# Optimization experiments

Measured on AMD Instinct MI355X. Metric: run time of the kernel, lower is better.

## Reference

```python
import jax, jax.numpy as jnp
import numpy as np

CELLS = 56
EPS = 1e-9

def setup_inputs() -> dict:
    key = jax.random.key(0)
    k1, k2 = jax.random.split(key)
    B = 512
    F = CELLS * CELLS * 15  # 47040 floats per sample
    output = jax.random.uniform(k1, (B, F), dtype=jnp.float32)
    target = jax.random.uniform(k2, (B, F), dtype=jnp.float32)
    return {"output": output, "target": target}

def reference(output, target):
    B = output.shape[0]
    # reshape flat vector into [B, cells^2, 15] slots: x,y,w,h,conf,classes[5:14]
    o = output.reshape(B, CELLS * CELLS, 15)
    t = target.reshape(B, CELLS * CELLS, 15)
    # coordinate loss: only x (slice [i*15 : i*15+1]) plus sqrt(w)/sqrt(h) terms
    coord = (o[..., 0] - t[..., 0]) ** 2 \
          + (jnp.sqrt(o[..., 2]) - jnp.sqrt(t[..., 2])) ** 2 \
          + (jnp.sqrt(o[..., 3]) - jnp.sqrt(t[..., 3])) ** 2
    # binary cross-entropy on confidence (slot 4)
    conf = -(t[..., 4] * jnp.log(o[..., 4] + EPS)
             + (1.0 - t[..., 4]) * jnp.log(1.0 - o[..., 4] + EPS))
    # class loss: sum of squared diffs over slots 5:14 (9 elements)
    cls = jnp.sum((t[..., 5:14] - o[..., 5:14]) ** 2, axis=-1)
    # cell is counted only if output x-coordinate is nonzero (torch.is_nonzero gate)
    mask = o[..., 0] != 0
    per_cell = jnp.where(mask, coord + conf + cls, 0.0)
    return jnp.sum(per_cell)
```

## Files before the change

### kernel.cpp

```cpp
#include <hip/hip_runtime.h>


#define EPSF 1e-9f
#define LN2F 0.69314718055994530942f

__device__ __forceinline__ float bce_of(float ox, float tx) {
    const float l1 = __log2f(ox + EPSF);
    const float l2 = __log2f((1.f - ox) + EPSF);
    return -LN2F * (tx * l1 + (1.f - tx) * l2);
}

__global__ __launch_bounds__(256, 4) void yolo_loss_fast(
    const float* __restrict__ o, const float* __restrict__ t,
    float* __restrict__ out_sum)
{
    const int tid = threadIdx.x;
    const unsigned T   = gridDim.x * 256u;
    const unsigned idx = blockIdx.x * 256u + (unsigned)tid;
    const float4* o4 = (const float4*)o;
    const float4* t4 = (const float4*)t;

    float4 ob[8], tb[8];
    float  gl[8], gh[8];
    unsigned sl[8];
    #pragma unroll
    for (int k = 0; k < 8; ++k) {
        const unsigned i  = idx + (unsigned)k * T;
        const unsigned e0 = i * 4u;
        const unsigned c0 = e0 / 15u;
        const unsigned c3 = (e0 + 3u) / 15u;
        sl[k] = e0 - c0 * 15u;
        ob[k] = o4[i];
        tb[k] = t4[i];
        gl[k] = o[c0 * 15u];
        gh[k] = o[c3 * 15u];
    }
    __builtin_amdgcn_sched_barrier(0);

    float acc = 0.f;
    #pragma unroll
    for (int k = 0; k < 8; ++k) {
        const unsigned s0 = sl[k];
        const float glo = gl[k], ghi = gh[k];
        const float oe[4] = {ob[k].x, ob[k].y, ob[k].z, ob[k].w};
        const float te[4] = {tb[k].x, tb[k].y, tb[k].z, tb[k].w};

        bool is4[4];
        #pragma unroll
        for (int j = 0; j < 4; ++j) {
            const unsigned s = s0 + (unsigned)j;
            is4[j] = (s == 4u) | (s == 19u);
        }
        float oc = oe[3], tc = te[3];
        #pragma unroll
        for (int j = 2; j >= 0; --j) { oc = is4[j] ? oe[j] : oc; tc = is4[j] ? te[j] : tc; }
        const float bce = bce_of(oc, tc);

        #pragma unroll
        for (int j = 0; j < 4; ++j) {
            unsigned s = s0 + (unsigned)j;
            const bool wrap = s >= 15u;
            s = wrap ? s - 15u : s;
            const float gate = wrap ? ghi : glo;
            const float ox = oe[j], tx = te[j];

            const float d  = ox - tx;
            const float sq = d * d;
            const float s23 = (ox + tx) - 2.f * __builtin_amdgcn_sqrtf(ox * tx);

            float c = ((s == 2u) | (s == 3u)) ? s23 : sq;
            c = is4[j] ? bce : c;
            c = ((s == 1u) | (s == 14u)) ? 0.f : c;
            c = (gate != 0.f) ? c : 0.f;
            acc += c;
        }
    }

    #pragma unroll
    for (int off = 32; off; off >>= 1) acc += __shfl_down(acc, off, 64);
    __shared__ float wsum[4];
    if ((tid & 63) == 0) wsum[tid >> 6] = acc;
    __syncthreads();
    if (tid == 0) atomicAdd(out_sum, wsum[0] + wsum[1] + wsum[2] + wsum[3]);
}

__global__ __launch_bounds__(256) void yolo_loss_generic(
    const float* __restrict__ o, const float* __restrict__ t,
    float* __restrict__ out_sum, int n4, int n)
{
    const int tid = threadIdx.x;
    const int stride = gridDim.x * 256;
    const float4* o4 = (const float4*)o;
    const float4* t4 = (const float4*)t;
    float acc = 0.f;

    for (int i = blockIdx.x * 256 + tid; i < n4; i += stride) {
        const float4 ov = o4[i];
        const float4 tv = t4[i];
        const unsigned e0 = (unsigned)i * 4u;
        const unsigned c0 = e0 / 15u;
        const unsigned c3 = (e0 + 3u) / 15u;
        const unsigned s0 = e0 - c0 * 15u;
        const float glo = o[c0 * 15u], ghi = o[c3 * 15u];
        const float oe[4] = {ov.x, ov.y, ov.z, ov.w};
        const float te[4] = {tv.x, tv.y, tv.z, tv.w};
        #pragma unroll
        for (int j = 0; j < 4; ++j) {
            unsigned s = s0 + (unsigned)j;
            const bool wrap = s >= 15u;
            s = wrap ? s - 15u : s;
            const float gate = wrap ? ghi : glo;
            const float ox = oe[j], tx = te[j];
            const float d = ox - tx;
            const float sq = d * d;
            const float s23 = (ox + tx) - 2.f * __builtin_amdgcn_sqrtf(ox * tx);
            float c = ((s == 2u) | (s == 3u)) ? s23 : sq;
            c = (s == 4u) ? bce_of(ox, tx) : c;
            c = ((s == 1u) | (s == 14u)) ? 0.f : c;
            c = (gate != 0.f) ? c : 0.f;
            acc += c;
        }
    }
    const int tail0 = n4 * 4;
    if (blockIdx.x == 0 && tid < n - tail0) {
        const unsigned e = (unsigned)(tail0 + tid);
        const unsigned cell = e / 15u;
        const unsigned s = e - cell * 15u;
        const float gate = o[cell * 15u];
        const float ox = o[e], tx = t[e];
        const float d = ox - tx;
        float c = d * d;
        c = ((s == 2u) | (s == 3u)) ? (ox + tx) - 2.f * __builtin_amdgcn_sqrtf(ox * tx) : c;
        c = (s == 4u) ? bce_of(ox, tx) : c;
        c = ((s == 1u) | (s == 14u)) ? 0.f : c;
        c = (gate != 0.f) ? c : 0.f;
        acc += c;
    }
    #pragma unroll
    for (int off = 32; off; off >>= 1) acc += __shfl_down(acc, off, 64);
    __shared__ float wsum[4];
    if ((tid & 63) == 0) wsum[tid >> 6] = acc;
    __syncthreads();
    if (tid == 0) atomicAdd(out_sum, wsum[0] + wsum[1] + wsum[2] + wsum[3]);
}

extern "C" void kernel_launch(void* const* d_in, const int* in_sizes, int n_in,
                              void* d_out, int out_size, void* d_ws, size_t ws_size,
                              hipStream_t stream) {
    const float* o = (const float*)d_in[0];
    const float* t = (const float*)d_in[1];
    float* out = (float*)d_out;
    const int n = in_sizes[0];
    const int n4 = n / 4;

    hipMemsetAsync(out, 0, sizeof(float), stream);

    if ((n % 4 == 0) && (n4 % (256 * 8) == 0)) {
        const int grid = n4 / (256 * 8);
        yolo_loss_fast<<<grid, 256, 0, stream>>>(o, t, out);
    } else {
        yolo_loss_generic<<<2940, 256, 0, stream>>>(o, t, out, n4, n);
    }
}
```

Before: 205.9 us.

## Map each wavefront to whole 15-float cells and fetch gates via shuffles

Each wavefront now processes windows of 60 float4s (240 floats, sixteen cells), so the per-lane slot pattern and cell boundaries are fixed and computed once per thread instead of per element. The scattered gate loads of each cell's x value are replaced by cross-lane shuffles from the lane that already holds that value. The grid is also fixed to 1792 blocks of 7 iterations with 7 waves per SIMD. The cost is that 4 of 64 lanes sit idle, and the fast path is tied to one exact input size.

```diff
diff --git a/kernel.cpp b/kernel.cpp
--- a/kernel.cpp
+++ b/kernel.cpp
@@ -3,6 +3,13 @@
 
 #define EPSF 1e-9f
 #define LN2F 0.69314718055994530942f
+
+#define GRID    1792
+#define KITERS  7
+#define BLK_E   (KITERS * 1920)
+#define FAST_N  (GRID * BLK_E)
+
+typedef float f32x4 __attribute__((ext_vector_type(4)));
 
 __device__ __forceinline__ float bce_of(float ox, float tx) {
     const float l1 = __log2f(ox + EPSF);
@@ -10,70 +17,85 @@
     return -LN2F * (tx * l1 + (1.f - tx) * l2);
 }
 
-__global__ __launch_bounds__(256, 4) void yolo_loss_fast(
+__global__ __launch_bounds__(256, 7) void yolo_loss_wave(
     const float* __restrict__ o, const float* __restrict__ t,
     float* __restrict__ out_sum)
 {
-    const int tid = threadIdx.x;
-    const unsigned T   = gridDim.x * 256u;
-    const unsigned idx = blockIdx.x * 256u + (unsigned)tid;
-    const float4* o4 = (const float4*)o;
-    const float4* t4 = (const float4*)t;
+    const int tid  = threadIdx.x;
+    const int lane = tid & 63;
+    const int wv   = tid >> 6;
+    const bool act = lane < 60;
 
-    float4 ob[8], tb[8];
-    float  gl[8], gh[8];
-    unsigned sl[8];
+    const f32x4* o4 = (const f32x4*)o;
+    const f32x4* t4 = (const f32x4*)t;
+
+    const unsigned le  = 4u * (unsigned)lane;
+    const unsigned c0r = le / 15u;
+    const unsigned c3r = (le + 3u) / 15u;
+    const unsigned s0  = le - c0r * 15u;
+    const int d_lo = (int)((15u * c0r) >> 2);
+    const int d_hi = (int)((15u * c3r) >> 2);
+    const unsigned j_own = (le + 14u) / 15u;
+    const unsigned gpos  = 15u * j_own - le;
+
+    bool is4[4], ksq[4], kz[4], wr[4];
     #pragma unroll
-    for (int k = 0; k < 8; ++k) {
-        const unsigned i  = idx + (unsigned)k * T;
-        const unsigned e0 = i * 4u;
-        const unsigned c0 = e0 / 15u;
-        const unsigned c3 = (e0 + 3u) / 15u;
-        sl[k] = e0 - c0 * 15u;
-        ob[k] = o4[i];
-        tb[k] = t4[i];
-        gl[k] = o[c0 * 15u];
-        gh[k] = o[c3 * 15u];
+    for (int j = 0; j < 4; ++j) {
+        const unsigned s = s0 + (unsigned)j;
+        is4[j] = (s == 4u);
+        ksq[j] = (s == 2u) | (s == 3u) | (s == 17u);
+        kz [j] = (s == 1u) | (s == 14u) | (s == 16u);
+        wr [j] = (s >= 15u);
     }
-    __builtin_amdgcn_sched_barrier(0);
 
-    float acc = 0.f;
-    #pragma unroll
-    for (int k = 0; k < 8; ++k) {
-        const unsigned s0 = sl[k];
-        const float glo = gl[k], ghi = gh[k];
-        const float oe[4] = {ob[k].x, ob[k].y, ob[k].z, ob[k].w};
-        const float te[4] = {tb[k].x, tb[k].y, tb[k].z, tb[k].w};
+    auto window_sum = [&](f32x4 ov, f32x4 tv) -> float {
+        const float gA   = (gpos & 1u) ? ov.y : ov.x;
+        const float gB   = (gpos & 1u) ? ov.w : ov.z;
+        const float gown = (gpos & 2u) ? gB : gA;
+        const float glo  = __shfl(gown, d_lo, 64);
+        const float ghi  = __shfl(gown, d_hi, 64);
 
-        bool is4[4];
-        #pragma unroll
-        for (int j = 0; j < 4; ++j) {
-            const unsigned s = s0 + (unsigned)j;
-            is4[j] = (s == 4u) | (s == 19u);
-        }
+        const float oe[4] = {ov.x, ov.y, ov.z, ov.w};
+        const float te[4] = {tv.x, tv.y, tv.z, tv.w};
+
         float oc = oe[3], tc = te[3];
         #pragma unroll
         for (int j = 2; j >= 0; --j) { oc = is4[j] ? oe[j] : oc; tc = is4[j] ? te[j] : tc; }
         const float bce = bce_of(oc, tc);
 
+        float sum = 0.f;
         #pragma unroll
         for (int j = 0; j < 4; ++j) {
-            unsigned s = s0 + (unsigned)j;
-            const bool wrap = s >= 15u;
-            s = wrap ? s - 15u : s;
-            const float gate = wrap ? ghi : glo;
+            const float gate = wr[j] ? ghi : glo;
             const float ox = oe[j], tx = te[j];
-
             const float d  = ox - tx;
             const float sq = d * d;
             const float s23 = (ox + tx) - 2.f * __builtin_amdgcn_sqrtf(ox * tx);
+            float c = ksq[j] ? s23 : sq;
+            c = is4[j] ? bce : c;
+            c = kz[j] ? 0.f : c;
+            c = (gate != 0.f) ? c : 0.f;
+            sum += c;
+        }
+        return sum;
+    };
 
-            float c = ((s == 2u) | (s == 3u)) ? s23 : sq;
-            c = is4[j] ? bce : c;
-            c = ((s == 1u) | (s == 14u)) ? 0.f : c;
-            c = (gate != 0.f) ? c : 0.f;
-            acc += c;
+    const unsigned blk_f4 = blockIdx.x * (unsigned)(BLK_E / 4);
+    float acc = 0.f;
+    #pragma unroll
+    for (int k = 0; k < KITERS; ++k) {
+        const unsigned wbase = blk_f4 + (unsigned)k * 480u + (unsigned)wv * 120u;
+        f32x4 ovA = {0.f,0.f,0.f,0.f}, tvA = {0.f,0.f,0.f,0.f};
+        f32x4 ovB = {0.f,0.f,0.f,0.f}, tvB = {0.f,0.f,0.f,0.f};
+        if (act) {
+            ovA = o4[wbase + (unsigned)lane];
+            tvA = t4[wbase + (unsigned)lane];
+            ovB = o4[wbase + 60u + (unsigned)lane];
+            tvB = t4[wbase + 60u + (unsigned)lane];
         }
+        const float sA = window_sum(ovA, tvA);
+        const float sB = window_sum(ovB, tvB);
+        acc += act ? (sA + sB) : 0.f;
     }
 
     #pragma unroll
@@ -151,14 +173,12 @@
     const float* t = (const float*)d_in[1];
     float* out = (float*)d_out;
     const int n = in_sizes[0];
-    const int n4 = n / 4;
 
     hipMemsetAsync(out, 0, sizeof(float), stream);
 
-    if ((n % 4 == 0) && (n4 % (256 * 8) == 0)) {
-        const int grid = n4 / (256 * 8);
-        yolo_loss_fast<<<grid, 256, 0, stream>>>(o, t, out);
+    if (n == FAST_N) {
+        yolo_loss_wave<<<GRID, 256, 0, stream>>>(o, t, out);
     } else {
-        yolo_loss_generic<<<2940, 256, 0, stream>>>(o, t, out, n4, n);
+        yolo_loss_generic<<<2940, 256, 0, stream>>>(o, t, out, n / 4, n);
     }
 }
```

New measurement: 261.5 us. 1.27x slower.
